# Kernel optimization log

Measured on AMD Instinct MI355X. Metric: run time of the kernel, lower is better.

The kernel has to match this reference:

```python
import jax, jax.numpy as jnp
import numpy as np

B = 4096   # batch
I = 1024   # in_features
O = 1024   # out_features
N = 4      # LUT fan-in; table size 2**N = 16


def setup_inputs() -> dict:
    key = jax.random.key(0)
    k1, k2, k3 = jax.random.split(key, 3)
    return {
        "x": jax.random.normal(k1, (B, I), dtype=jnp.float32),
        # learnable mapping logits: (out_features, n, in_features)
        "mapping_logits": jax.random.normal(k2, (O, N, I), dtype=jnp.float32),
        # per-node LUT tables with 2**n corner values each
        "lut_tables": jax.random.normal(k3, (O, 2 ** N), dtype=jnp.float32),
    }


def reference(x, mapping_logits, lut_tables):
    # softmax-weighted input selection: (B,I) x (O,N,I) -> (B,O,N)
    w = jax.nn.softmax(mapping_logits, axis=-1)
    selected = jnp.einsum('bi,oni->bon', x, w)
    # BatchedLUTNodes: squash to [0,1], multilinear interpolation over 2**N corners
    s = jax.nn.sigmoid(selected)                      # (B,O,N)
    cw = jnp.ones(s.shape[:2] + (1,), dtype=s.dtype)  # corner weights, grows to (B,O,2**N)
    for j in range(N):                                # fixed small loop over fan-in
        sj = s[..., j][..., None]                     # (B,O,1)
        cw = jnp.concatenate([cw * (1.0 - sj), cw * sj], axis=-1)
    # weighted sum of per-node table entries -> (B,O)
    return jnp.einsum('boc,oc->bo', cw, lut_tables)
```

## Files before the change

### kernel.cpp

```cpp
#include <hip/hip_runtime.h>

#define B_DIM 4096
#define I_DIM 1024
#define O_DIM 1024
#define ON_DIM 4096
#define TILE_HALFS 4096

typedef _Float16 half8  __attribute__((ext_vector_type(8)));
typedef _Float16 half4_t __attribute__((ext_vector_type(4)));
typedef float    floatx4 __attribute__((ext_vector_type(4)));

__global__ __launch_bounds__(256)
void ltn_prep(const float* __restrict__ logits, const float* __restrict__ x,
              _Float16* __restrict__ wt, _Float16* __restrict__ xt) {
  const int t = threadIdx.x;
  if (blockIdx.x < 1024) {
    __shared__ _Float16 lbuf[4][1040];
    const int lane = t & 63, wv = t >> 6;
    const int row  = blockIdx.x * 4 + wv;
    const int nb   = row >> 7;
    const int nnB  = (blockIdx.x * 4) & 127;
    const float4* s4 = (const float4*)(logits + (size_t)row * I_DIM);
    float4 v[4];
#pragma unroll
    for (int j = 0; j < 4; j++) v[j] = s4[lane * 4 + j];
    float m = -1e30f;
#pragma unroll
    for (int j = 0; j < 4; j++)
      m = fmaxf(m, fmaxf(fmaxf(v[j].x, v[j].y), fmaxf(v[j].z, v[j].w)));
#pragma unroll
    for (int off = 1; off < 64; off <<= 1) m = fmaxf(m, __shfl_xor(m, off));
    float s = 0.0f;
#pragma unroll
    for (int j = 0; j < 4; j++) {
      v[j].x = __expf(v[j].x - m); v[j].y = __expf(v[j].y - m);
      v[j].z = __expf(v[j].z - m); v[j].w = __expf(v[j].w - m);
      s += v[j].x + v[j].y + v[j].z + v[j].w;
    }
#pragma unroll
    for (int off = 1; off < 64; off <<= 1) s += __shfl_xor(s, off);
    const float inv = 1.0f / s;
#pragma unroll
    for (int j = 0; j < 4; j++) {
      half4_t h;
      h[0] = (_Float16)(v[j].x * inv); h[1] = (_Float16)(v[j].y * inv);
      h[2] = (_Float16)(v[j].z * inv); h[3] = (_Float16)(v[j].w * inv);
      *(half4_t*)&lbuf[wv][lane * 16 + j * 4] = h;
    }
    __syncthreads();
#pragma unroll
    for (int p = 0; p < 2; p++) {
      const int u   = t + p * 256;
      const int nn4 = u & 3;
      const int kb8 = (u >> 2) & 3;
      const int kb  = u >> 4;
      const half8 h = *(const half8*)&lbuf[nn4][kb * 32 + kb8 * 8];
      _Float16* dst = wt + ((size_t)nb * 32 + kb) * TILE_HALFS
                    + kb8 * 1024 + (nnB + nn4) * 8;
      *(half8*)dst = h;
    }
  } else {
    const int bid = blockIdx.x - 1024;
    const int nn = t >> 1;
    const int hf = t & 1;
    const int mb = bid >> 5, kt = bid & 31;
    const int row = mb * 128 + nn;
    const float4* src = (const float4*)(x + (size_t)row * I_DIM + kt * 32 + hf * 16);
    const float4 a = src[0], b = src[1], c = src[2], d = src[3];
    half8 h0, h1;
    h0[0] = (_Float16)a.x; h0[1] = (_Float16)a.y; h0[2] = (_Float16)a.z; h0[3] = (_Float16)a.w;
    h0[4] = (_Float16)b.x; h0[5] = (_Float16)b.y; h0[6] = (_Float16)b.z; h0[7] = (_Float16)b.w;
    h1[0] = (_Float16)c.x; h1[1] = (_Float16)c.y; h1[2] = (_Float16)c.z; h1[3] = (_Float16)c.w;
    h1[4] = (_Float16)d.x; h1[5] = (_Float16)d.y; h1[6] = (_Float16)d.z; h1[7] = (_Float16)d.w;
    _Float16* base = xt + ((size_t)mb * 32 + kt) * TILE_HALFS + (hf * 2) * 1024 + nn * 8;
    *(half8*)base = h0;
    *(half8*)(base + 1024) = h1;
  }
}

__global__ __launch_bounds__(512, 2)
void ltn_gemm_lut(const _Float16* __restrict__ xt,
                  const _Float16* __restrict__ wt,
                  const float* __restrict__ lut,
                  float* __restrict__ out) {
  __shared__ _Float16 sm[3 * 16384];

  const int tid  = threadIdx.x;
  const int lane = tid & 63;
  const int wv   = tid >> 6;
  const int wr   = wv >> 1;
  const int wc   = wv & 1;

  const int id  = blockIdx.x;
  const int xcd = id & 7;
  const int li  = id >> 3;
  const int mb  = (xcd & 3) * 4 + (li & 3);
  const int nb  = (xcd >> 2) * 8 + (li >> 2);

  const int fm = lane & 15;
  const int kq = lane >> 4;

  const size_t baseA = (size_t)(mb * 2) * 32 * TILE_HALFS;
  const size_t baseB = (size_t)(nb * 2) * 32 * TILE_HALFS;

  floatx4 acc[4][8];
#pragma unroll
  for (int i = 0; i < 4; i++)
#pragma unroll
    for (int j = 0; j < 8; j++) acc[i][j] = (floatx4)0.0f;

  auto stage = [&](int bufOff , int kt) {
#pragma unroll
    for (int s = 0; s < 4; s++) {
      const int c   = wv * 4 + s;
      const int cc  = c & 15;
      const int tl  = cc >> 3;
      const int sub = cc & 7;
      const _Float16* g;
      int dst;
      if (c < 16) {
        g = xt + baseA + (size_t)(tl * 32 + kt) * TILE_HALFS + sub * 512 + lane * 8;
        dst = bufOff + cc * 512;
      } else {
        g = wt + baseB + (size_t)(tl * 32 + kt) * TILE_HALFS + sub * 512 + lane * 8;
        dst = bufOff + 8192 + cc * 512;
      }
      __builtin_amdgcn_global_load_lds(
          (const __attribute__((address_space(1))) void*)g,
          (__attribute__((address_space(3))) void*)(sm + dst), 16, 0, 0);
    }
  };

  auto compute = [&](int bufOff) {
    half8 af[4], bf[8];
#pragma unroll
    for (int f = 0; f < 4; f++)
      af[f] = *(const half8*)&sm[bufOff + ((wr >> 1) * 4 + kq) * 1024
                                 + ((wr & 1) * 64 + f * 16 + fm) * 8];
#pragma unroll
    for (int g = 0; g < 8; g++)
      bf[g] = *(const half8*)&sm[bufOff + 8192 + (wc * 4 + kq) * 1024
                                 + (g * 16 + fm) * 8];
    __builtin_amdgcn_s_setprio(1);
#pragma unroll
    for (int mt = 0; mt < 4; mt++)
#pragma unroll
      for (int nt = 0; nt < 8; nt++)
        acc[mt][nt] = __builtin_amdgcn_mfma_f32_16x16x32_f16(
            af[mt], bf[nt], acc[mt][nt], 0, 0, 0);
    __builtin_amdgcn_s_setprio(0);
  };

  stage(0, 0);
  stage(16384, 1);
  int o0 = 0, o1 = 16384, o2 = 32768;

#pragma unroll 1
  for (int kt = 0; kt < 32; kt++) {
    if (kt < 31) asm volatile("s_waitcnt vmcnt(4)" ::: "memory");
    else         asm volatile("s_waitcnt vmcnt(0)" ::: "memory");
    __builtin_amdgcn_s_barrier();
    __builtin_amdgcn_sched_barrier(0);
    if (kt + 2 < 32) stage(o2, kt + 2);
    compute(o0);
    const int t0 = o0; o0 = o1; o1 = o2; o2 = t0;
  }

#pragma unroll
  for (int nt = 0; nt < 8; nt++) {
    const int o = (nb * 256 + wc * 128 + nt * 16 + fm) >> 2;
    const float4* lt4 = (const float4*)(lut + (size_t)o * 16);
    const float4 L0 = lt4[0], L1 = lt4[1], L2 = lt4[2], L3 = lt4[3];
#pragma unroll
    for (int mt = 0; mt < 4; mt++) {
#pragma unroll
      for (int r = 0; r < 4; r++) {
        const float v  = acc[mt][nt][r];
        const float sv = 1.0f / (1.0f + __expf(-v));
        const float s1 = __shfl_down(sv, 1);
        const float s2 = __shfl_down(sv, 2);
        const float s3 = __shfl_down(sv, 3);
        if ((lane & 3) == 0) {
          const float s0 = sv;
          const float a0 = L0.x + (L2.x - L0.x) * s3;
          const float a1 = L0.y + (L2.y - L0.y) * s3;
          const float a2 = L0.z + (L2.z - L0.z) * s3;
          const float a3 = L0.w + (L2.w - L0.w) * s3;
          const float a4 = L1.x + (L3.x - L1.x) * s3;
          const float a5 = L1.y + (L3.y - L1.y) * s3;
          const float a6 = L1.z + (L3.z - L1.z) * s3;
          const float a7 = L1.w + (L3.w - L1.w) * s3;
          const float b0 = a0 + (a4 - a0) * s2;
          const float b1 = a1 + (a5 - a1) * s2;
          const float b2 = a2 + (a6 - a2) * s2;
          const float b3 = a3 + (a7 - a3) * s2;
          const float c0 = b0 + (b2 - b0) * s1;
          const float c1 = b1 + (b3 - b1) * s1;
          const float res = c0 + (c1 - c0) * s0;
          const int row = mb * 256 + wr * 64 + mt * 16 + (lane >> 4) * 4 + r;
          out[(size_t)row * O_DIM + o] = res;
        }
      }
    }
  }
}

extern "C" void kernel_launch(void* const* d_in, const int* in_sizes, int n_in,
                              void* d_out, int out_size, void* d_ws, size_t ws_size,
                              hipStream_t stream) {
  const float* x      = (const float*)d_in[0];
  const float* logits = (const float*)d_in[1];
  const float* lut    = (const float*)d_in[2];
  float* out          = (float*)d_out;

  _Float16* wt = (_Float16*)d_ws;
  _Float16* xt = (_Float16*)d_ws + (size_t)ON_DIM * I_DIM;

  ltn_prep<<<2048, 256, 0, stream>>>(logits, x, wt, xt);
  ltn_gemm_lut<<<256, 512, 0, stream>>>(xt, wt, lut, out);
}
```

Baseline: 132.8 us.

## Give each wave private LDS B tiles and register-load A fragments without barriers

Restructures the GEMM main loop so each wave stages its own B tile into a private LDS slice and loads its A fragments straight from global memory into double-buffered registers. This removes the block-wide s_barrier per K-step and the shared LDS staging of A. In exchange, B tiles are no longer shared across waves and A fragments are no longer shared through LDS, so global/L2 traffic rises. LDS use per block also grows to 128KB, which limits residency to one block per CU.

```diff
diff --git a/kernel.cpp b/kernel.cpp
--- a/kernel.cpp
+++ b/kernel.cpp
@@ -83,7 +83,7 @@
                   const _Float16* __restrict__ wt,
                   const float* __restrict__ lut,
                   float* __restrict__ out) {
-  __shared__ _Float16 sm[3 * 16384];
+  __shared__ _Float16 sm[8 * 8192];
 
   const int tid  = threadIdx.x;
   const int lane = tid & 63;
@@ -100,8 +100,12 @@
   const int fm = lane & 15;
   const int kq = lane >> 4;
 
-  const size_t baseA = (size_t)(mb * 2) * 32 * TILE_HALFS;
-  const size_t baseB = (size_t)(nb * 2) * 32 * TILE_HALFS;
+  const _Float16* xA = xt + (size_t)(mb * 2 + (wr >> 1)) * 32 * TILE_HALFS;
+  const int ro = (wr & 1) * 64;
+  const int laneA = kq * 1024 + (ro + fm) * 8;
+  const _Float16* wB = wt + (size_t)(nb * 2 + wc) * 32 * TILE_HALFS;
+  const int laneB = kq * 1024 + fm * 8;
+  _Float16* myB = sm + wv * 8192;
 
   floatx4 acc[4][8];
 #pragma unroll
@@ -109,38 +113,42 @@
 #pragma unroll
     for (int j = 0; j < 8; j++) acc[i][j] = (floatx4)0.0f;
 
-  auto stage = [&](int bufOff , int kt) {
-#pragma unroll
-    for (int s = 0; s < 4; s++) {
-      const int c   = wv * 4 + s;
-      const int cc  = c & 15;
-      const int tl  = cc >> 3;
-      const int sub = cc & 7;
-      const _Float16* g;
-      int dst;
-      if (c < 16) {
-        g = xt + baseA + (size_t)(tl * 32 + kt) * TILE_HALFS + sub * 512 + lane * 8;
-        dst = bufOff + cc * 512;
-      } else {
-        g = wt + baseB + (size_t)(tl * 32 + kt) * TILE_HALFS + sub * 512 + lane * 8;
-        dst = bufOff + 8192 + cc * 512;
-      }
+  auto stageB = [&](int buf, int kt) {
+    const _Float16* img = wB + (size_t)kt * TILE_HALFS;
+#pragma unroll
+    for (int c = 0; c < 8; c++) {
       __builtin_amdgcn_global_load_lds(
-          (const __attribute__((address_space(1))) void*)g,
-          (__attribute__((address_space(3))) void*)(sm + dst), 16, 0, 0);
+          (const __attribute__((address_space(1))) void*)(img + c * 512 + lane * 8),
+          (__attribute__((address_space(3))) void*)(myB + buf * 4096 + c * 512),
+          16, 0, 0);
     }
   };
 
-  auto compute = [&](int bufOff) {
-    half8 af[4], bf[8];
+  half8 afA[4], afB[4];
+  auto loadA = [&](half8 (&af)[4], int kt) {
+    const _Float16* img = xA + (size_t)kt * TILE_HALFS;
 #pragma unroll
     for (int f = 0; f < 4; f++)
-      af[f] = *(const half8*)&sm[bufOff + ((wr >> 1) * 4 + kq) * 1024
-                                 + ((wr & 1) * 64 + f * 16 + fm) * 8];
+      af[f] = *(const half8*)(img + laneA + f * 128);
+  };
+
+  stageB(0, 0);
+  stageB(1, 1);
+  loadA(afA, 0);
+  loadA(afB, 1);
+
+  auto body = [&](int kt, half8 (&af)[4], int buf) {
+    if (kt < 30) asm volatile("s_waitcnt vmcnt(12)" ::: "memory");
+    else         asm volatile("s_waitcnt vmcnt(0)"  ::: "memory");
+    __builtin_amdgcn_sched_barrier(0);
+    half8 bf[8];
 #pragma unroll
     for (int g = 0; g < 8; g++)
-      bf[g] = *(const half8*)&sm[bufOff + 8192 + (wc * 4 + kq) * 1024
-                                 + (g * 16 + fm) * 8];
+      bf[g] = *(const half8*)(myB + buf * 4096 + laneB + g * 128);
+    asm volatile("s_waitcnt lgkmcnt(0)" ::: "memory");
+    __builtin_amdgcn_sched_barrier(0);
+    if (kt + 2 < 32) stageB(buf, kt + 2);
+    __builtin_amdgcn_sched_barrier(0);
     __builtin_amdgcn_s_setprio(1);
 #pragma unroll
     for (int mt = 0; mt < 4; mt++)
@@ -149,21 +157,14 @@
         acc[mt][nt] = __builtin_amdgcn_mfma_f32_16x16x32_f16(
             af[mt], bf[nt], acc[mt][nt], 0, 0, 0);
     __builtin_amdgcn_s_setprio(0);
+    if (kt + 2 < 32) loadA(af, kt + 2);
+    __builtin_amdgcn_sched_barrier(0);
   };
 
-  stage(0, 0);
-  stage(16384, 1);
-  int o0 = 0, o1 = 16384, o2 = 32768;
-
 #pragma unroll 1
-  for (int kt = 0; kt < 32; kt++) {
-    if (kt < 31) asm volatile("s_waitcnt vmcnt(4)" ::: "memory");
-    else         asm volatile("s_waitcnt vmcnt(0)" ::: "memory");
-    __builtin_amdgcn_s_barrier();
-    __builtin_amdgcn_sched_barrier(0);
-    if (kt + 2 < 32) stage(o2, kt + 2);
-    compute(o0);
-    const int t0 = o0; o0 = o1; o1 = o2; o2 = t0;
+  for (int k2 = 0; k2 < 16; k2++) {
+    body(2 * k2,     afA, 0);
+    body(2 * k2 + 1, afB, 1);
   }
 
 #pragma unroll
```

Measured after the change: 135.0 us. No clear change (+1.6%).
